# Optimization experiments

Measured on AMD Instinct MI355X. Metric: run time of the kernel, lower is better.

## Reference

```python
import jax, jax.numpy as jnp
import numpy as np

DIM_MODEL = 2048
DQK = 64
DV = 64
NUM_HEADS = 32
NUM_GROUPS = 8
H_PER_G = NUM_HEADS // NUM_GROUPS
ROPE_THETA = 10000.0
RMS_EPS = 1e-6


def _rope(x):
    # x: [b, g, h, s, d]; rotate-half RoPE over last dim, positions along s.
    d = x.shape[-1]
    s = x.shape[-2]
    inv_freq = 1.0 / (ROPE_THETA ** (jnp.arange(0, d, 2, dtype=jnp.float32) / d))  # [d/2]
    ang = jnp.arange(s, dtype=jnp.float32)[:, None] * inv_freq[None, :]  # [s, d/2]
    cos, sin = jnp.cos(ang), jnp.sin(ang)
    x1, x2 = x[..., : d // 2], x[..., d // 2 :]
    return jnp.concatenate([x1 * cos - x2 * sin, x2 * cos + x1 * sin], axis=-1)


def setup_inputs() -> dict:
    key = jax.random.key(0)
    k1, k2, k3 = jax.random.split(key, 3)
    b, s = 2, 2048
    concat = NUM_HEADS * DQK + NUM_GROUPS * (DQK + DV)  # 3072
    x = jax.random.normal(k1, (b, s, DIM_MODEL), dtype=jnp.float32)
    w_in = jax.random.normal(k2, (concat, DIM_MODEL), dtype=jnp.float32) * (DIM_MODEL ** -0.5)
    w_out = jax.random.normal(k3, (DIM_MODEL, NUM_HEADS * DV), dtype=jnp.float32) * ((NUM_HEADS * DV) ** -0.5)
    rms_w = jnp.ones((DIM_MODEL,), dtype=jnp.float32)
    return {"x": x, "w_in": w_in, "w_out": w_out, "rms_w": rms_w}


def reference(x, w_in, w_out, rms_w):
    b, s, _ = x.shape
    # RMSNorm
    y = x * jax.lax.rsqrt(jnp.mean(x * x, axis=-1, keepdims=True) + RMS_EPS) * rms_w
    # In-projection (Linear, no bias): y @ w_in.T
    y = jnp.einsum('bsm,cm->bsc', y, w_in)
    cq = NUM_HEADS * DQK
    ck = NUM_GROUPS * DQK
    q, k, v = y[..., :cq], y[..., cq:cq + ck], y[..., cq + ck:]
    # q: b s (g h d) -> b g h s d ; k,v: b s (g d) -> b g 1 s d
    q = q.reshape(b, s, NUM_GROUPS, H_PER_G, DQK).transpose(0, 2, 3, 1, 4)
    k = k.reshape(b, s, NUM_GROUPS, DQK).transpose(0, 2, 1, 3)[:, :, None]
    v = v.reshape(b, s, NUM_GROUPS, DV).transpose(0, 2, 1, 3)[:, :, None]
    q = _rope(q)
    k = _rope(k)
    # scores with GQA broadcast over h
    qk = jnp.einsum('bghsd,bgxpd->bghsp', q, k) * (DQK ** -0.5)
    causal = jnp.tril(jnp.ones((s, s), dtype=bool))
    qk = jnp.where(causal, qk, -jnp.inf)
    attn = jax.nn.softmax(qk, axis=-1)
    o = jnp.einsum('bghsp,bgxpd->bghsd', attn, v)  # [b,g,h,s,d]
    o = o.transpose(0, 3, 1, 2, 4).reshape(b, s, NUM_HEADS * DV)
    y = jnp.einsum('bsc,mc->bsm', o, w_out)
    return x + y
```

## Files before the change

### kernel.cpp

```cpp
#include <hip/hip_runtime.h>
#include <hip/hip_bf16.h>

#define TOKENS   4096
#define SEQ      2048
#define DMODEL   2048
#define CONCAT   3072
#define NHEADS   32
#define NGROUPS  8
#define HPERG    4
#define CQ       2048
#define CK       512

typedef __attribute__((ext_vector_type(8))) short bf16x8;
typedef __attribute__((ext_vector_type(4))) float f32x4;

__device__ __forceinline__ ushort f2bf(float f) {
    __hip_bfloat16 h = __float2bfloat16(f);
    return __builtin_bit_cast(ushort, h);
}

#define GLOBAL_TO_LDS16(g, l)                                                  \
    __builtin_amdgcn_global_load_lds(                                          \
        (const __attribute__((address_space(1))) void*)(g),                    \
        (__attribute__((address_space(3))) void*)(l), 16, 0, 0)

__global__ void rmsnorm_kernel(const float* __restrict__ x,
                               const float* __restrict__ w,
                               ushort* __restrict__ y_bf) {
    int t = blockIdx.x;
    const float4* xr = (const float4*)(x + (size_t)t * DMODEL);
    float4 v[2];
    float ss = 0.f;
#pragma unroll
    for (int i = 0; i < 2; i++) {
        v[i] = xr[threadIdx.x + i * 256];
        ss += v[i].x * v[i].x + v[i].y * v[i].y + v[i].z * v[i].z + v[i].w * v[i].w;
    }
#pragma unroll
    for (int off = 32; off >= 1; off >>= 1) ss += __shfl_xor(ss, off);
    __shared__ float red[4];
    int wid = threadIdx.x >> 6;
    if ((threadIdx.x & 63) == 0) red[wid] = ss;
    __syncthreads();
    float total = red[0] + red[1] + red[2] + red[3];
    float scale = rsqrtf(total * (1.0f / DMODEL) + 1e-6f);
    const float4* wr = (const float4*)w;
    ushort4* yr = (ushort4*)(y_bf + (size_t)t * DMODEL);
#pragma unroll
    for (int i = 0; i < 2; i++) {
        int c = threadIdx.x + i * 256;
        float4 wv = wr[c];
        ushort4 o;
        o.x = f2bf(v[i].x * scale * wv.x);
        o.y = f2bf(v[i].y * scale * wv.y);
        o.z = f2bf(v[i].z * scale * wv.z);
        o.w = f2bf(v[i].w * scale * wv.w);
        yr[c] = o;
    }
}

__global__ void pack_bf16_kernel(const float* __restrict__ src,
                                 ushort* __restrict__ dst, int n4) {
    int i = blockIdx.x * 256 + threadIdx.x;
    if (i < n4) {
        float4 v = ((const float4*)src)[i];
        ushort4 o;
        o.x = f2bf(v.x); o.y = f2bf(v.y); o.z = f2bf(v.z); o.w = f2bf(v.w);
        ((ushort4*)dst)[i] = o;
    }
}

#define LGKM(nn) asm volatile("s_waitcnt lgkmcnt(" #nn ")" ::: "memory")
#define VMC(nn)  asm volatile("s_waitcnt vmcnt(" #nn ")" ::: "memory")
#define SBAR()   __builtin_amdgcn_s_barrier()
#define SCHED0() __builtin_amdgcn_sched_barrier(0)
#define PRIO(p)  __builtin_amdgcn_s_setprio(p)

#define RD_A(mh)                                                              \
    _Pragma("unroll") for (int mi = 0; mi < 4; mi++)                          \
    _Pragma("unroll") for (int ks = 0; ks < 2; ks++)                          \
        af[mi][ks] = *(const bf16x8*)(Ab +                                    \
            ((arow0 + (mh) * 64 + mi * 16) * 8 +                              \
             ((ks * 4 + quad) ^ an)) * 8);

#define RD_B(nh)                                                              \
    _Pragma("unroll") for (int ni = 0; ni < NFRAG; ni++)                      \
    _Pragma("unroll") for (int ks = 0; ks < 2; ks++)                          \
        bfr[nh][ni][ks] = *(const bf16x8*)(Bb +                               \
            ((brow0 + (nh) * (16 * NFRAG) + ni * 16) * 8 +                    \
             ((ks * 4 + quad) ^ an)) * 8);

#define MMQ(mh, nh)                                                           \
    _Pragma("unroll") for (int mi = 0; mi < 4; mi++)                          \
    _Pragma("unroll") for (int ni = 0; ni < NFRAG; ni++)                      \
    _Pragma("unroll") for (int ks = 0; ks < 2; ks++)                          \
        acc[(mh) * 4 + mi][(nh) * NFRAG + ni] =                               \
            __builtin_amdgcn_mfma_f32_16x16x32_bf16(af[mi][ks],               \
                bfr[nh][ni][ks], acc[(mh) * 4 + mi][(nh) * NFRAG + ni],       \
                0, 0, 0);

#define ISSUE_HALF(H_)                                                        \
    {                                                                         \
        int H = (H_);                                                         \
        if (H < 4 * NT) {                                                     \
            int t2 = H >> 2, j2 = H & 3;                                      \
            int k0 = t2 << 6;                                                 \
            if (j2 == 0 || j2 == 3) {                                         \
                int half = (j2 == 3);                                         \
                ushort* lb = (ushort*)&As[t2 & 1][0];                         \
                _Pragma("unroll") for (int c = 0; c < 2; c++) {               \
                    int s = w * 2 + c;                                        \
                    int row = (s >> 3) * 128 + half * 64 + (s & 7) * 8;       \
                    const ushort* g = Aptr +                                  \
                        (size_t)(bm + row + l8) * K + k0 + kb8;               \
                    GLOBAL_TO_LDS16(g, lb + row * 64);                        \
                }                                                             \
            } else {                                                          \
                int half = (j2 == 2);                                         \
                ushort* lb = (ushort*)&Bs[t2 & 1][0];                         \
                if constexpr (NFRAG == 2) {                                   \
                    _Pragma("unroll") for (int c = 0; c < 2; c++) {           \
                        int s = w * 2 + c;                                    \
                        int row = (s >> 2) * 64 + half * 32 + (s & 3) * 8;    \
                        const ushort* g = Bptr +                              \
                            (size_t)(bn + row + l8) * K + k0 + kb8;           \
                        GLOBAL_TO_LDS16(g, lb + row * 64);                    \
                    }                                                         \
                } else {                                                      \
                    int row = (w >> 1) * 32 + half * 16 + (w & 1) * 8;        \
                    const ushort* g = Bptr +                                  \
                        (size_t)(bn + row + l8) * K + k0 + kb8;               \
                    GLOBAL_TO_LDS16(g, lb + row * 64);                        \
                }                                                             \
            }                                                                 \
        }                                                                     \
    }

#define VMC_STEADY()                                                          \
    { if constexpr (NFRAG == 2) { VMC(6); } else { VMC(4); } }

#define TILE(t_, BUF)                                                         \
    {                                                                         \
        const ushort* Ab = &As[BUF][0];                                       \
        const ushort* Bb = &Bs[BUF][0];                                       \
                                                \
        RD_A(0); RD_B(0);                                                     \
        ISSUE_HALF(4 * (t_) + 7);                                             \
        LGKM(8);                                                              \
        SBAR(); LGKM(0); SCHED0();                                            \
        PRIO(1); MMQ(0, 0); PRIO(0);                                          \
        SBAR();                                                               \
                                                   \
        RD_B(1);                                                              \
        ISSUE_HALF(4 * (t_) + 8);                                             \
        SBAR(); LGKM(0); SCHED0();                                            \
        PRIO(1); MMQ(0, 1); PRIO(0);                                          \
        SBAR();                                                               \
                                                   \
        RD_A(1);                                                              \
        ISSUE_HALF(4 * (t_) + 9);                                             \
        SBAR(); LGKM(0); SCHED0();                                            \
        PRIO(1); MMQ(1, 0); PRIO(0);                                          \
        SBAR();                                                               \
                           \
        ISSUE_HALF(4 * (t_) + 10);                                            \
        SBAR(); SCHED0();                                                     \
        PRIO(1); MMQ(1, 1); PRIO(0);                                          \
        if ((t_) + 2 < NT)        { VMC_STEADY(); }                           \
        else if ((t_) + 2 == NT)  { VMC(0); }                                 \
        SBAR();                                                               \
    }

template <bool EPILOGUE, int NFRAG>
__global__ __launch_bounds__(512, 2) void gemm_nt_8ph(
        const ushort* __restrict__ Aptr, const ushort* __restrict__ Bptr,
        float* __restrict__ C, const float* __restrict__ X,
        float* __restrict__ OUT, int M, int N, int K) {
    __shared__ __align__(16) ushort As[2][256 * 64];
    __shared__ __align__(16) ushort Bs[2][NFRAG * 128 * 64];

    const int bm = blockIdx.y * 256, bn = blockIdx.x * (128 * NFRAG);
    const int w = threadIdx.x >> 6, lane = threadIdx.x & 63;
    const int n = lane & 15, quad = lane >> 4;
    const int wm = w >> 2, wn = w & 3;
    const int an = n & 7;
    const int l8 = lane >> 3;
    const int kb8 = ((lane & 7) ^ l8) * 8;
    const int arow0 = wm * 128 + n;
    const int brow0 = wn * (32 * NFRAG) + n;
    const int NT = K >> 6;

    f32x4 acc[8][2 * NFRAG] = {};
    bf16x8 af[4][2], bfr[2][NFRAG][2];

    ISSUE_HALF(0); ISSUE_HALF(1); ISSUE_HALF(2); ISSUE_HALF(3);
    ISSUE_HALF(4); ISSUE_HALF(5); ISSUE_HALF(6);
    VMC_STEADY();
    SBAR();

    for (int tt = 0; tt < NT; tt += 2) {
        TILE(tt, 0);
        TILE(tt + 1, 1);
    }

#pragma unroll
    for (int mi = 0; mi < 8; mi++)
#pragma unroll
        for (int ni = 0; ni < 2 * NFRAG; ni++) {
            int row = bm + wm * 128 + mi * 16 + quad * 4;
            int col = bn + wn * (32 * NFRAG) + ni * 16 + n;
#pragma unroll
            for (int r = 0; r < 4; r++) {
                size_t idx = (size_t)(row + r) * N + col;
                float v = acc[mi][ni][r];
                if (EPILOGUE) OUT[idx] = X[idx] + v;
                else          C[idx]   = v;
            }
        }
}

__global__ void pack_qk_kernel(const float* __restrict__ qkv,
                               __hip_bfloat16* __restrict__ Qb,
                               __hip_bfloat16* __restrict__ Kb) {
    int t = blockIdx.x;
    int b = t >> 11, s = t & (SEQ - 1);
    const float* row = qkv + (size_t)t * CONCAT;
    const float LOG2_THETA = 13.287712379549449f;
    const float QSCALE = 0.18033688011112042f;
    for (int i = threadIdx.x; i < CQ + CK; i += 256) {
        int head, d;
        const float* hb;
        if (i < CQ) { head = i >> 6; d = i & 63; hb = row + head * 64; }
        else { head = (i - CQ) >> 6; d = (i - CQ) & 63; hb = row + CQ + head * 64; }
        int j = d & 31;
        float inv = exp2f(-((float)j / 32.0f) * LOG2_THETA);
        float ang = (float)s * inv;
        float c = cosf(ang), sn = sinf(ang);
        float val;
        if (d < 32) val = hb[d] * c - hb[d + 32] * sn;
        else        val = hb[d] * c + hb[d - 32] * sn;
        if (i < CQ) val *= QSCALE;
        __hip_bfloat16 bv = __float2bfloat16(val);
        if (i < CQ) {
            int g = head >> 2, h = head & 3;
            Qb[((size_t)((b * 8 + g) * 4 + h) * SEQ + s) * 64 + d] = bv;
        } else {
            Kb[((size_t)(b * 8 + head) * SEQ + s) * 64 + d] = bv;
        }
    }
}

__global__ void pack_v_kernel(const float* __restrict__ qkv,
                              __hip_bfloat16* __restrict__ Vb) {
    int st = blockIdx.x & 31, bg = blockIdx.x >> 5;
    int b = bg >> 3, g = bg & 7;
    __shared__ float tile[64][65];
    int tid = threadIdx.x;
    int ls = tid >> 6;
    int d = tid & 63;
#pragma unroll
    for (int i = 0; i < 16; i++) {
        int s = st * 64 + i * 4 + ls;
        tile[i * 4 + ls][d] = qkv[(size_t)(b * SEQ + s) * CONCAT + CQ + CK + g * 64 + d];
    }
    __syncthreads();
#pragma unroll
    for (int i = 0; i < 16; i++) {
        int drow = i * 4 + ls;
        int scol = tid & 63;
        Vb[((size_t)(bg * 64 + drow)) * SEQ + st * 64 + scol] =
            __float2bfloat16(tile[scol][drow]);
    }
}

#define AISSUE(kt_, buf_)                                                     \
    {                                                                         \
        const ushort* Kg_ = Kg0 + (kt_) * 64 * 64;                            \
        const ushort* Vg_ = Vg0 + (kt_) * 64;                                 \
        _Pragma("unroll") for (int r_ = 0; r_ < 2; r_++) {                    \
            GLOBAL_TO_LDS16(Kg_ + (r_ * 32 + w * 8) * 64 + koff,              \
                            &Kl[buf_][(r_ * 256 + w * 64) * 8]);              \
            GLOBAL_TO_LDS16(Vg_ + (size_t)(r_ * 32 + w * 8) * SEQ + voff,     \
                            &Vl[buf_][(r_ * 256 + w * 64) * 8]);              \
        }                                                                     \
    }

__global__ __launch_bounds__(256) void attn_mfma_kernel(
        const ushort* __restrict__ Qb, const ushort* __restrict__ Kb,
        const ushort* __restrict__ Vb, ushort* __restrict__ o_bf) {
    __shared__ __align__(16) ushort Kl[2][512 * 8];
    __shared__ __align__(16) ushort Vl[2][512 * 8];
    __shared__ __align__(16) uint   Pl[4][1056];

    int blk = blockIdx.x;
    int qt  = 15 - (blk >> 6);
    int bgh = blk & 63;
    int h = bgh & 3, g = (bgh >> 2) & 7, b = bgh >> 5;
    int w = threadIdx.x >> 6, lane = threadIdx.x & 63;
    int n = lane & 15, quad = lane >> 4;
    const int an = n & 7;
    int Q0 = qt * 128;
    int qw = Q0 + w * 32;

    const int l3 = lane >> 3;
    const int lx = (lane & 7) ^ l3;
    const int koff = l3 * 64 + lx * 8;
    const int voff = l3 * SEQ + lx * 8;

    const ushort* Qh  = Qb + (size_t)((b * 8 + g) * 4 + h) * (SEQ * 64);
    const ushort* Kg0 = Kb + (size_t)(b * 8 + g) * (SEQ * 64);
    const ushort* Vg0 = Vb + (size_t)(b * 8 + g) * (64 * SEQ);

    bf16x8 aq[2][2];
#pragma unroll
    for (int qg = 0; qg < 2; qg++)
#pragma unroll
        for (int ks = 0; ks < 2; ks++)
            aq[qg][ks] = *(const bf16x8*)(
                Qh + (size_t)(qw + qg * 16 + n) * 64 + ks * 32 + quad * 8);

    f32x4 od[2][4] = {};
    f32x4 od4[2] = {};

    short onev = (n == 0) ? (short)0x3F80 : (short)0;
    bf16x8 bones = {onev, onev, onev, onev, onev, onev, onev, onev};

    uint* Pw = Pl[w];
    int nkt = qt * 2 + 2;

    AISSUE(0, 0);
    AISSUE(1, 1);

    for (int kt = 0; kt < nkt; kt++) {
        int buf = kt & 1;
        if (kt + 1 < nkt) { VMC(4); } else { VMC(0); }
        SBAR(); SCHED0();

        bool act1 = (kt * 64 <= qw + 31);
        if (act1) {
            bool act0 = (kt * 64 <= qw + 15);
            const ushort* Kb_ = Kl[buf];
            const ushort* Vb_ = Vl[buf];

#pragma unroll
            for (int t16k = 0; t16k < 4; t16k++) {
                int krow = (t16k * 16 + n) * 8;
                bf16x8 kf0 = *(const bf16x8*)(Kb_ + (krow + (quad ^ an)) * 8);
                bf16x8 kf1 = *(const bf16x8*)(Kb_ + (krow + ((quad + 4) ^ an)) * 8);
                int key0 = kt * 64 + t16k * 16 + quad * 4;
#pragma unroll
                for (int qg = 0; qg < 2; qg++) {
                    if (qg == 0 && !act0) continue;
                    f32x4 c = {};
                    c = __builtin_amdgcn_mfma_f32_16x16x32_bf16(kf0, aq[qg][0], c, 0, 0, 0);
                    c = __builtin_amdgcn_mfma_f32_16x16x32_bf16(kf1, aq[qg][1], c, 0, 0, 0);
                    int qrow = qw + qg * 16 + n;
                    float p[4];
                    if (kt * 64 + 63 > qw + qg * 16) {
#pragma unroll
                        for (int r = 0; r < 4; r++)
                            p[r] = (key0 + r <= qrow) ? __builtin_amdgcn_exp2f(c[r]) : 0.f;
                    } else {
#pragma unroll
                        for (int r = 0; r < 4; r++)
                            p[r] = __builtin_amdgcn_exp2f(c[r]);
                    }
                    uint d0 = ((uint)f2bf(p[1]) << 16) | f2bf(p[0]);
                    uint d1 = ((uint)f2bf(p[3]) << 16) | f2bf(p[2]);
                    int base = ((t16k * 2 + (quad >> 1)) * 33 + qg * 16 + n) * 4
                               + (quad & 1) * 2;
                    Pw[base]     = d0;
                    Pw[base + 1] = d1;
                }
            }

#pragma unroll
            for (int kb2 = 0; kb2 < 2; kb2++) {
                int kb = kb2 * 4 + quad;
                bf16x8 bv[4];
#pragma unroll
                for (int dt = 0; dt < 4; dt++)
                    bv[dt] = *(const bf16x8*)(Vb_ +
                        (((dt * 16 + n) * 8 + (kb ^ an)) * 8));
#pragma unroll
                for (int qg = 0; qg < 2; qg++) {
                    if (qg == 0 && !act0) continue;
                    bf16x8 ap = *(const bf16x8*)(
                        (const ushort*)Pw + ((kb2 * 4 + quad) * 33 + qg * 16 + n) * 8);
#pragma unroll
                    for (int dt = 0; dt < 4; dt++)
                        od[qg][dt] = __builtin_amdgcn_mfma_f32_16x16x32_bf16(
                            ap, bv[dt], od[qg][dt], 0, 0, 0);
                    od4[qg] = __builtin_amdgcn_mfma_f32_16x16x32_bf16(
                        ap, bones, od4[qg], 0, 0, 0);
                }
            }
        }

        SCHED0(); SBAR();
        if (kt + 2 < nkt) AISSUE(kt + 2, buf);
    }

#pragma unroll
    for (int qg = 0; qg < 2; qg++) {
        float linv[4];
#pragma unroll
        for (int r = 0; r < 4; r++) {
            float lv = __shfl(od4[qg][r], lane & 48);
            linv[r] = __builtin_amdgcn_rcpf(lv);
        }
#pragma unroll
        for (int dt = 0; dt < 4; dt++)
#pragma unroll
            for (int r = 0; r < 4; r++) {
                int q = qw + qg * 16 + quad * 4 + r;
                int col = (g * 4 + h) * 64 + dt * 16 + n;
                o_bf[(size_t)(b * SEQ + q) * DMODEL + col] =
                    f2bf(od[qg][dt][r] * linv[r]);
            }
    }
}

extern "C" void kernel_launch(void* const* d_in, const int* in_sizes, int n_in,
                              void* d_out, int out_size, void* d_ws, size_t ws_size,
                              hipStream_t stream) {
    const float* x     = (const float*)d_in[0];
    const float* w_in  = (const float*)d_in[1];
    const float* w_out = (const float*)d_in[2];
    const float* rms_w = (const float*)d_in[3];
    float* out = (float*)d_out;

    const size_t MB = 1024 * 1024;
    char* ws = (char*)d_ws;
    float*  qkv      = (float*)ws;
    ushort* y_bf     = (ushort*)(ws + 48 * MB);
    ushort* w_in_bf  = (ushort*)(ws + 64 * MB);
    ushort* Qb       = (ushort*)(ws + 48 * MB);
    ushort* Kb       = (ushort*)(ws + 64 * MB);
    ushort* Vb       = (ushort*)(ws + 68 * MB);
    ushort* o_bf     = (ushort*)ws;
    ushort* w_out_bf = (ushort*)(ws + 16 * MB);

    rmsnorm_kernel<<<TOKENS, 256, 0, stream>>>(x, rms_w, y_bf);
    pack_bf16_kernel<<<(CONCAT * DMODEL / 4 + 255) / 256, 256, 0, stream>>>(
        w_in, w_in_bf, CONCAT * DMODEL / 4);

    gemm_nt_8ph<false, 2><<<dim3(CONCAT / 256, TOKENS / 256), 512, 0, stream>>>(
        y_bf, w_in_bf, qkv, nullptr, nullptr, TOKENS, CONCAT, DMODEL);

    pack_qk_kernel<<<TOKENS, 256, 0, stream>>>(qkv, (__hip_bfloat16*)Qb,
                                               (__hip_bfloat16*)Kb);
    pack_v_kernel<<<512, 256, 0, stream>>>(qkv, (__hip_bfloat16*)Vb);
    pack_bf16_kernel<<<(DMODEL * DMODEL / 4 + 255) / 256, 256, 0, stream>>>(
        w_out, w_out_bf, DMODEL * DMODEL / 4);

    attn_mfma_kernel<<<1024, 256, 0, stream>>>(Qb, Kb, Vb, o_bf);

    gemm_nt_8ph<true, 1><<<dim3(DMODEL / 128, TOKENS / 256), 512, 0, stream>>>(
        o_bf, w_out_bf, nullptr, x, out, TOKENS, DMODEL, DMODEL);
}
```

Measured before the change: 317.8 us.

## Swizzle GEMM workgroup order and fuse Q/K/V pack kernels with shared RoPE tables

The GEMM now remaps its linear workgroup index with a stride-8 swizzle, so consecutive workgroups are spread across chiplets/XCDs to improve cache locality of the A/B tiles. The separate Q/K and V pack kernels are merged into one launch that uses branch-by-block-index. The Q/K path computes RoPE cos/sin once per token into shared memory and handles each rotation pair per thread, instead of recomputing exp2/cos/sin per element. The changes risk a different L2 access pattern and extra shared-memory use in the fused kernel.

```diff
diff --git a/kernel.cpp b/kernel.cpp
--- a/kernel.cpp
+++ b/kernel.cpp
@@ -179,7 +179,13 @@
     __shared__ __align__(16) ushort As[2][256 * 64];
     __shared__ __align__(16) ushort Bs[2][NFRAG * 128 * 64];
 
-    const int bm = blockIdx.y * 256, bn = blockIdx.x * (128 * NFRAG);
+    int nwg = (int)(gridDim.x * gridDim.y);
+    int lin = (int)(blockIdx.y * gridDim.x + blockIdx.x);
+    int swz = lin;
+    if ((nwg & 7) == 0) swz = (lin & 7) * (nwg >> 3) + (lin >> 3);
+    const int bm = (swz / (int)gridDim.x) * 256;
+    const int bn = (swz % (int)gridDim.x) * (128 * NFRAG);
+
     const int w = threadIdx.x >> 6, lane = threadIdx.x & 63;
     const int n = lane & 15, quad = lane >> 4;
     const int wm = w >> 2, wn = w & 3;
@@ -219,57 +225,69 @@
         }
 }
 
-__global__ void pack_qk_kernel(const float* __restrict__ qkv,
-                               __hip_bfloat16* __restrict__ Qb,
-                               __hip_bfloat16* __restrict__ Kb) {
-    int t = blockIdx.x;
-    int b = t >> 11, s = t & (SEQ - 1);
-    const float* row = qkv + (size_t)t * CONCAT;
-    const float LOG2_THETA = 13.287712379549449f;
-    const float QSCALE = 0.18033688011112042f;
-    for (int i = threadIdx.x; i < CQ + CK; i += 256) {
-        int head, d;
-        const float* hb;
-        if (i < CQ) { head = i >> 6; d = i & 63; hb = row + head * 64; }
-        else { head = (i - CQ) >> 6; d = (i - CQ) & 63; hb = row + CQ + head * 64; }
-        int j = d & 31;
-        float inv = exp2f(-((float)j / 32.0f) * LOG2_THETA);
-        float ang = (float)s * inv;
-        float c = cosf(ang), sn = sinf(ang);
-        float val;
-        if (d < 32) val = hb[d] * c - hb[d + 32] * sn;
-        else        val = hb[d] * c + hb[d - 32] * sn;
-        if (i < CQ) val *= QSCALE;
-        __hip_bfloat16 bv = __float2bfloat16(val);
-        if (i < CQ) {
-            int g = head >> 2, h = head & 3;
-            Qb[((size_t)((b * 8 + g) * 4 + h) * SEQ + s) * 64 + d] = bv;
-        } else {
-            Kb[((size_t)(b * 8 + head) * SEQ + s) * 64 + d] = bv;
-        }
-    }
-}
-
-__global__ void pack_v_kernel(const float* __restrict__ qkv,
-                              __hip_bfloat16* __restrict__ Vb) {
-    int st = blockIdx.x & 31, bg = blockIdx.x >> 5;
-    int b = bg >> 3, g = bg & 7;
+__global__ void pack_qkv_kernel(const float* __restrict__ qkv,
+                                ushort* __restrict__ Qb,
+                                ushort* __restrict__ Kb,
+                                ushort* __restrict__ Vb) {
+    __shared__ float cs[32], sn[32];
     __shared__ float tile[64][65];
     int tid = threadIdx.x;
-    int ls = tid >> 6;
-    int d = tid & 63;
-#pragma unroll
-    for (int i = 0; i < 16; i++) {
-        int s = st * 64 + i * 4 + ls;
-        tile[i * 4 + ls][d] = qkv[(size_t)(b * SEQ + s) * CONCAT + CQ + CK + g * 64 + d];
-    }
-    __syncthreads();
-#pragma unroll
-    for (int i = 0; i < 16; i++) {
-        int drow = i * 4 + ls;
-        int scol = tid & 63;
-        Vb[((size_t)(bg * 64 + drow)) * SEQ + st * 64 + scol] =
-            __float2bfloat16(tile[scol][drow]);
+
+    if (blockIdx.x < TOKENS) {
+        int t = blockIdx.x;
+        int b = t >> 11, s = t & (SEQ - 1);
+        const float* row = qkv + (size_t)t * CONCAT;
+        if (tid < 32) {
+            const float LOG2_THETA = 13.287712379549449f;
+            float inv = exp2f(-((float)tid / 32.0f) * LOG2_THETA);
+            float ang = (float)s * inv;
+            cs[tid] = cosf(ang);
+            sn[tid] = sinf(ang);
+        }
+        __syncthreads();
+        const float QSCALE = 0.18033688011112042f;
+#pragma unroll
+        for (int it = 0; it < (CQ + CK) / 2 / 256; it++) {
+            int p = tid + it * 256;
+            int head = p >> 5, j = p & 31;
+            const float* hb = row + head * 64;
+            float x1 = hb[j], x2 = hb[j + 32];
+            float c = cs[j], s2 = sn[j];
+            float o1 = x1 * c - x2 * s2;
+            float o2 = x2 * c + x1 * s2;
+            if (head < 32) {
+                o1 *= QSCALE; o2 *= QSCALE;
+                int g = head >> 2, h = head & 3;
+                ushort* q = Qb + ((size_t)((b * 8 + g) * 4 + h) * SEQ + s) * 64;
+                q[j]      = f2bf(o1);
+                q[j + 32] = f2bf(o2);
+            } else {
+                int kh = head - 32;
+                ushort* kk = Kb + ((size_t)(b * 8 + kh) * SEQ + s) * 64;
+                kk[j]      = f2bf(o1);
+                kk[j + 32] = f2bf(o2);
+            }
+        }
+    } else {
+        int bid = blockIdx.x - TOKENS;
+        int st = bid & 31, bg = bid >> 5;
+        int b = bg >> 3, g = bg & 7;
+        int ls = tid >> 6;
+        int d = tid & 63;
+#pragma unroll
+        for (int i = 0; i < 16; i++) {
+            int s = st * 64 + i * 4 + ls;
+            tile[i * 4 + ls][d] =
+                qkv[(size_t)(b * SEQ + s) * CONCAT + CQ + CK + g * 64 + d];
+        }
+        __syncthreads();
+#pragma unroll
+        for (int i = 0; i < 16; i++) {
+            int drow = i * 4 + ls;
+            int scol = tid & 63;
+            Vb[((size_t)(bg * 64 + drow)) * SEQ + st * 64 + scol] =
+                f2bf(tile[scol][drow]);
+        }
     }
 }
 
@@ -448,9 +466,8 @@
     gemm_nt_8ph<false, 2><<<dim3(CONCAT / 256, TOKENS / 256), 512, 0, stream>>>(
         y_bf, w_in_bf, qkv, nullptr, nullptr, TOKENS, CONCAT, DMODEL);
 
-    pack_qk_kernel<<<TOKENS, 256, 0, stream>>>(qkv, (__hip_bfloat16*)Qb,
-                                               (__hip_bfloat16*)Kb);
-    pack_v_kernel<<<512, 256, 0, stream>>>(qkv, (__hip_bfloat16*)Vb);
+    pack_qkv_kernel<<<TOKENS + 512, 256, 0, stream>>>(
+        qkv, Qb, Kb, Vb);
     pack_bf16_kernel<<<(DMODEL * DMODEL / 4 + 255) / 256, 256, 0, stream>>>(
         w_out, w_out_bf, DMODEL * DMODEL / 4);
 
```

Measured after the change: 300.9 us. -5.3%, faster.
